# Optimization experiments

Measured on AMD Instinct MI355X. Metric: run time of the kernel, lower is better.

## Reference

```python
import jax, jax.numpy as jnp
import numpy as np

BLOCK = 64  # bitsandbytes 4-bit blocksize
OUT, IN = 4096, 4096
# NF4 codebook (bitsandbytes values)
NF4_CODE = np.array([
    -1.0, -0.6961928009986877, -0.5250730514526367, -0.39491748809814453,
    -0.28444138169288635, -0.18477343022823334, -0.09105003625154495, 0.0,
    0.07958029955625534, 0.16093020141124725, 0.24611230194568634,
    0.33791524171829224, 0.44070982933044434, 0.5626170039176941,
    0.7229568362236023, 1.0], dtype=np.float32)


def setup_inputs() -> dict:
    key = jax.random.key(0)
    k1, k2, k3 = jax.random.split(key, 3)
    x = jax.random.normal(k1, (8, 2048, IN), dtype=jnp.float32)
    qweight = jax.random.randint(k2, (OUT * IN,), 0, 16, dtype=jnp.int32)
    absmax = jax.random.uniform(k3, (OUT * IN // BLOCK,), dtype=jnp.float32)
    return {"x": x, "qweight": qweight, "absmax": absmax}


def reference(x, qweight, absmax):
    code = jnp.asarray(NF4_CODE)
    # dequantize: codebook lookup, then per-block absmax scaling
    w = code[qweight].reshape(-1, BLOCK) * absmax[:, None]  # [n_blocks, BLOCK]
    W = w.reshape(OUT, IN)                                   # [out, in]
    # linear: y = x @ W^T  (no bias: quantized_bias is None)
    return jnp.einsum('bsi,oi->bso', x, W)
```

## Files before the change

### kernel.cpp

```cpp
#include <hip/hip_runtime.h>
#include <hip/hip_bf16.h>
#include <stdint.h>

#define IN_DIM  4096
#define OUT_DIM 4096
#define M_DIM   16384
#define BK      64
#define NT      (IN_DIM / BK)

typedef float f32x4 __attribute__((ext_vector_type(4)));
typedef short bf16x8 __attribute__((ext_vector_type(8)));
typedef short bf16x4 __attribute__((ext_vector_type(4)));
typedef int   i32x4 __attribute__((ext_vector_type(4)));

__device__ __constant__ float NF4_CODE_D[16] = {
    -1.0f, -0.6961928009986877f, -0.5250730514526367f, -0.39491748809814453f,
    -0.28444138169288635f, -0.18477343022823334f, -0.09105003625154495f, 0.0f,
    0.07958029955625534f, 0.16093020141124725f, 0.24611230194568634f,
    0.33791524171829224f, 0.44070982933044434f, 0.5626170039176941f,
    0.7229568362236023f, 1.0f};

static __device__ __forceinline__ ushort f2bf(float f) {
  union { float f; uint32_t u; } v; v.f = f;
  uint32_t r = v.u + 0x7FFFu + ((v.u >> 16) & 1u);
  return (ushort)(r >> 16);
}

__global__ void dequant_nf4(const int* __restrict__ q, const float* __restrict__ am,
                            ushort* __restrict__ w) {
  __shared__ float code[16];
  if (threadIdx.x < 16) code[threadIdx.x] = NF4_CODE_D[threadIdx.x];
  __syncthreads();
  size_t t = (size_t)blockIdx.x * blockDim.x + threadIdx.x;
  size_t base = t * 8;
  i32x4 qa = *(const i32x4*)(q + base);
  i32x4 qb = *(const i32x4*)(q + base + 4);
  float s = am[base >> 6];
  bf16x8 o;
  o[0] = (short)f2bf(code[qa[0] & 15] * s);
  o[1] = (short)f2bf(code[qa[1] & 15] * s);
  o[2] = (short)f2bf(code[qa[2] & 15] * s);
  o[3] = (short)f2bf(code[qa[3] & 15] * s);
  o[4] = (short)f2bf(code[qb[0] & 15] * s);
  o[5] = (short)f2bf(code[qb[1] & 15] * s);
  o[6] = (short)f2bf(code[qb[2] & 15] * s);
  o[7] = (short)f2bf(code[qb[3] & 15] * s);
  *(bf16x8*)(w + base) = o;
}

__global__ void cvt_x(const float* __restrict__ x, ushort* __restrict__ xb) {
  size_t t = (size_t)blockIdx.x * blockDim.x + threadIdx.x;
  size_t base = t * 8;
  f32x4 a = *(const f32x4*)(x + base);
  f32x4 b = *(const f32x4*)(x + base + 4);
  bf16x8 o;
  o[0] = (short)f2bf(a[0]); o[1] = (short)f2bf(a[1]);
  o[2] = (short)f2bf(a[2]); o[3] = (short)f2bf(a[3]);
  o[4] = (short)f2bf(b[0]); o[5] = (short)f2bf(b[1]);
  o[6] = (short)f2bf(b[2]); o[7] = (short)f2bf(b[3]);
  *(bf16x8*)(xb + base) = o;
}

static __device__ __forceinline__ void llds16(const ushort* g, ushort* l) {
  __builtin_amdgcn_global_load_lds(
      (const __attribute__((address_space(1))) void*)g,
      (__attribute__((address_space(3))) void*)l, 16, 0, 0);
}

__global__ __launch_bounds__(512, 2) void gemm256(const ushort* __restrict__ Xb,
                                                  const ushort* __restrict__ W,
                                                  float* __restrict__ Y) {
  __shared__ ushort As[2][256 * BK];
  __shared__ ushort Bs[2][256 * BK];

  const int tid  = threadIdx.x;
  const int lane = tid & 63;
  const int wid  = tid >> 6;
  const int wr   = wid >> 2;
  const int wc   = wid & 3;
  const int l15  = lane & 15;
  const int kg   = lane >> 4;
  const int l7   = lane & 7;

  const int bid = blockIdx.x;
  const int wg  = (bid & 7) * 128 + (bid >> 3);
  const int tm  = wg >> 4;
  const int tn  = wg & 15;
  const size_t row0 = (size_t)tm * 256;
  const size_t col0 = (size_t)tn * 256;

  const int srow  = tid >> 3;
  const int scol8 = ((tid & 7) ^ (srow & 7)) * 8;
  const int wbase = wid << 9;

  f32x4  acc[8][4] = {};
  bf16x8 aA[4][2], aB[4][2], b0[2][2], b1[2][2];

#define BARX()   asm volatile("s_barrier" ::: "memory")
#define LGKM0()  do { asm volatile("s_waitcnt lgkmcnt(0)" ::: "memory"); \
                      __builtin_amdgcn_sched_barrier(0); } while (0)
#define LGKM8()  asm volatile("s_waitcnt lgkmcnt(8)" ::: "memory")
#define VMC(n)   asm volatile("s_waitcnt vmcnt(" #n ")" ::: "memory")
#define PRI1()   __builtin_amdgcn_s_setprio(1)
#define PRI0()   __builtin_amdgcn_s_setprio(0)

#define STAGE_A(kt, h, nb) do { \
    llds16(Xb + (row0 + (h)*128 +  0 + srow) * IN_DIM + (kt)*BK + scol8, \
           &As[nb][(h)*8192 +    0 + wbase]); \
    llds16(Xb + (row0 + (h)*128 + 64 + srow) * IN_DIM + (kt)*BK + scol8, \
           &As[nb][(h)*8192 + 4096 + wbase]); \
  } while (0)

#define STAGE_B(kt, h, nb) do { \
    llds16(W + (col0 + (h)*128 +  0 + srow) * IN_DIM + (kt)*BK + scol8, \
           &Bs[nb][(h)*8192 +    0 + wbase]); \
    llds16(W + (col0 + (h)*128 + 64 + srow) * IN_DIM + (kt)*BK + scol8, \
           &Bs[nb][(h)*8192 + 4096 + wbase]); \
  } while (0)

#define LDA_(dst, nb, mh) do { \
    _Pragma("unroll") for (int mi = 0; mi < 4; ++mi) \
    _Pragma("unroll") for (int ks = 0; ks < 2; ++ks) \
      dst[mi][ks] = *(const bf16x8*)&As[nb][((mh)*128 + wr*64 + mi*16 + l15) * BK \
                                            + (((ks*4 + kg) ^ l7) * 8)]; \
  } while (0)

#define LDB_(dst, nb, nh) do { \
    _Pragma("unroll") for (int ni = 0; ni < 2; ++ni) \
    _Pragma("unroll") for (int ks = 0; ks < 2; ++ks) \
      dst[ni][ks] = *(const bf16x8*)&Bs[nb][((nh)*128 + wc*32 + ni*16 + l15) * BK \
                                            + (((ks*4 + kg) ^ l7) * 8)]; \
  } while (0)

#define QUAD(mh, nh, aR, bR) do { PRI1(); \
    _Pragma("unroll") for (int mi = 0; mi < 4; ++mi) \
    _Pragma("unroll") for (int ni = 0; ni < 2; ++ni) \
    _Pragma("unroll") for (int ks = 0; ks < 2; ++ks) \
      acc[(mh)*4 + mi][(nh)*2 + ni] = __builtin_amdgcn_mfma_f32_16x16x32_bf16( \
          aR[mi][ks], bR[ni][ks], acc[(mh)*4 + mi][(nh)*2 + ni], 0, 0, 0); \
    PRI0(); } while (0)

  STAGE_A(0, 0, 0); STAGE_B(0, 0, 0); STAGE_A(0, 1, 0); STAGE_B(0, 1, 0);
  STAGE_A(1, 0, 1); STAGE_B(1, 0, 1); STAGE_A(1, 1, 1); STAGE_B(1, 1, 1);
  VMC(8); BARX();
  LDA_(aA, 0, 0); LDB_(b0, 0, 0);

#pragma unroll 1
  for (int t = 0; t < NT - 2; ++t) {
    const int cur = t & 1, nxt = cur ^ 1;
    LDA_(aB, cur, 1);
    STAGE_A(t + 2, 0, cur);
    BARX(); LGKM0();
    QUAD(0, 0, aA, b0);
    BARX();
    LDB_(b1, cur, 1);
    STAGE_B(t + 2, 0, cur);
    BARX(); LGKM0();
    QUAD(1, 0, aB, b0);
    BARX();
    STAGE_A(t + 2, 1, cur);
    VMC(10);
    BARX(); LGKM0();
    QUAD(0, 1, aA, b1);
    BARX();
    LDA_(aA, nxt, 0); LDB_(b0, nxt, 0);
    STAGE_B(t + 2, 1, cur);
    LGKM8();
    VMC(8);
    BARX(); LGKM0();
    QUAD(1, 1, aB, b1);
    BARX();
  }

  LDA_(aB, 0, 1);
  BARX(); LGKM0();
  QUAD(0, 0, aA, b0);
  BARX();
  LDB_(b1, 0, 1);
  BARX(); LGKM0();
  QUAD(1, 0, aB, b0);
  BARX();
  VMC(4);
  BARX(); LGKM0();
  QUAD(0, 1, aA, b1);
  BARX();
  LDA_(aA, 1, 0); LDB_(b0, 1, 0);
  LGKM8(); VMC(0);
  BARX(); LGKM0();
  QUAD(1, 1, aB, b1);
  BARX();

  LDA_(aB, 1, 1); LDB_(b1, 1, 1);
  QUAD(0, 0, aA, b0);
  QUAD(1, 0, aB, b0);
  QUAD(0, 1, aA, b1);
  QUAD(1, 1, aB, b1);

#undef QUAD
#undef LDB_
#undef LDA_
#undef STAGE_B
#undef STAGE_A

  float* yb = Y + (row0 + wr * 64 + kg * 4) * OUT_DIM + col0 + wc * 32 + l15;
#pragma unroll
  for (int mh = 0; mh < 2; ++mh)
#pragma unroll
    for (int mi = 0; mi < 4; ++mi)
#pragma unroll
      for (int nh = 0; nh < 2; ++nh)
#pragma unroll
        for (int ni = 0; ni < 2; ++ni)
#pragma unroll
          for (int v = 0; v < 4; ++v)
            yb[(size_t)(mh * 128 + mi * 16 + v) * OUT_DIM + nh * 128 + ni * 16] =
                acc[mh * 4 + mi][nh * 2 + ni][v];
}

__global__ void gemm_fb(const float* __restrict__ X, const ushort* __restrict__ W,
                        float* __restrict__ Y) {
  __shared__ ushort Af[128 * 64];
  __shared__ ushort Bf[128 * 64];
  const int tid  = threadIdx.x;
  const int lane = tid & 63;
  const int wid  = tid >> 6;
  const int wr   = wid >> 1, wc = wid & 1;
  const int bid  = blockIdx.x;
  const int tm   = bid / 32, tn = bid % 32;
  const size_t row0 = (size_t)tm * 128, col0 = (size_t)tn * 128;
  f32x4 acc[4][4] = {};
  const int arow = lane & 15, kgrp = lane >> 4;
  const int srow = lane >> 3, scol = (lane & 7) * 8;
  for (int k0 = 0; k0 < IN_DIM; k0 += 64) {
    f32x4 r[8];
#pragma unroll
    for (int i = 0; i < 8; ++i)
      r[i] = *(const f32x4*)(X + (row0 + i * 16 + (tid >> 4)) * IN_DIM + k0 + (tid & 15) * 4);
#pragma unroll
    for (int i = 0; i < 8; ++i) {
      bf16x4 o;
      o[0] = (short)f2bf(r[i][0]); o[1] = (short)f2bf(r[i][1]);
      o[2] = (short)f2bf(r[i][2]); o[3] = (short)f2bf(r[i][3]);
      *(bf16x4*)&Af[(i * 16 + (tid >> 4)) * 64 + (tid & 15) * 4] = o;
    }
#pragma unroll
    for (int i = 0; i < 4; ++i) {
      const int c = wid * 4 + i;
      llds16(W + (col0 + c * 8 + srow) * IN_DIM + k0 + scol, Bf + c * 512);
    }
    __syncthreads();
#pragma unroll
    for (int ks = 0; ks < 2; ++ks) {
      bf16x8 a[4], b[4];
#pragma unroll
      for (int m = 0; m < 4; ++m)
        a[m] = *(const bf16x8*)&Af[(wr * 64 + m * 16 + arow) * 64 + ks * 32 + kgrp * 8];
#pragma unroll
      for (int n = 0; n < 4; ++n)
        b[n] = *(const bf16x8*)&Bf[(wc * 64 + n * 16 + arow) * 64 + ks * 32 + kgrp * 8];
#pragma unroll
      for (int m = 0; m < 4; ++m)
#pragma unroll
        for (int n = 0; n < 4; ++n)
          acc[m][n] = __builtin_amdgcn_mfma_f32_16x16x32_bf16(a[m], b[n], acc[m][n], 0, 0, 0);
    }
    __syncthreads();
  }
  float* yb = Y + (row0 + wr * 64) * OUT_DIM + col0 + wc * 64;
  const int crow = (lane >> 4) * 4, ccol = lane & 15;
#pragma unroll
  for (int m = 0; m < 4; ++m)
#pragma unroll
    for (int n = 0; n < 4; ++n)
#pragma unroll
      for (int v = 0; v < 4; ++v)
        yb[(size_t)(m * 16 + crow + v) * OUT_DIM + n * 16 + ccol] = acc[m][n][v];
}

extern "C" void kernel_launch(void* const* d_in, const int* in_sizes, int n_in,
                              void* d_out, int out_size, void* d_ws, size_t ws_size,
                              hipStream_t stream) {
  const float* x  = (const float*)d_in[0];
  const int*   q  = (const int*)d_in[1];
  const float* am = (const float*)d_in[2];
  float* y = (float*)d_out;

  ushort* w = (ushort*)d_ws;
  const size_t WB = (size_t)OUT_DIM * IN_DIM * sizeof(ushort);
  const size_t XB = (size_t)M_DIM * IN_DIM * sizeof(ushort);

  dequant_nf4<<<(OUT_DIM * (size_t)IN_DIM) / 8 / 256, 256, 0, stream>>>(q, am, w);

  if (ws_size >= WB + XB) {
    ushort* xb = (ushort*)((char*)d_ws + WB);
    cvt_x<<<((size_t)M_DIM * IN_DIM) / 8 / 256, 256, 0, stream>>>(x, xb);
    gemm256<<<(M_DIM / 256) * (OUT_DIM / 256), 512, 0, stream>>>(xb, w, y);
  } else {
    gemm_fb<<<(M_DIM / 128) * (OUT_DIM / 128), 256, 0, stream>>>(x, w, y);
  }
}
```

Baseline: 616.3 us.

## Merge dequant and x-convert kernels, reschedule GEMM main-loop LDS/stage order

Combines the NF4 dequantization and fp32-to-bf16 conversion of x into one prep kernel, selected by block index, which removes a launch and lets the two phases overlap. It also reorders the GEMM main loop so that the four MFMA quadrants run in the order (0,0),(0,1),(1,0),(1,1). Fragment loads from LDS are moved into the current iteration, and the last B stage of the next tile is issued inside the loop, with adjusted vmcnt waits. The new schedule changes how global-to-LDS staging overlaps with compute, and it needs the wait counts to stay correct to avoid races.

```diff
diff --git a/kernel.cpp b/kernel.cpp
--- a/kernel.cpp
+++ b/kernel.cpp
@@ -26,39 +26,41 @@
   return (ushort)(r >> 16);
 }
 
-__global__ void dequant_nf4(const int* __restrict__ q, const float* __restrict__ am,
-                            ushort* __restrict__ w) {
-  __shared__ float code[16];
-  if (threadIdx.x < 16) code[threadIdx.x] = NF4_CODE_D[threadIdx.x];
-  __syncthreads();
-  size_t t = (size_t)blockIdx.x * blockDim.x + threadIdx.x;
-  size_t base = t * 8;
-  i32x4 qa = *(const i32x4*)(q + base);
-  i32x4 qb = *(const i32x4*)(q + base + 4);
-  float s = am[base >> 6];
-  bf16x8 o;
-  o[0] = (short)f2bf(code[qa[0] & 15] * s);
-  o[1] = (short)f2bf(code[qa[1] & 15] * s);
-  o[2] = (short)f2bf(code[qa[2] & 15] * s);
-  o[3] = (short)f2bf(code[qa[3] & 15] * s);
-  o[4] = (short)f2bf(code[qb[0] & 15] * s);
-  o[5] = (short)f2bf(code[qb[1] & 15] * s);
-  o[6] = (short)f2bf(code[qb[2] & 15] * s);
-  o[7] = (short)f2bf(code[qb[3] & 15] * s);
-  *(bf16x8*)(w + base) = o;
-}
-
-__global__ void cvt_x(const float* __restrict__ x, ushort* __restrict__ xb) {
-  size_t t = (size_t)blockIdx.x * blockDim.x + threadIdx.x;
-  size_t base = t * 8;
-  f32x4 a = *(const f32x4*)(x + base);
-  f32x4 b = *(const f32x4*)(x + base + 4);
-  bf16x8 o;
-  o[0] = (short)f2bf(a[0]); o[1] = (short)f2bf(a[1]);
-  o[2] = (short)f2bf(a[2]); o[3] = (short)f2bf(a[3]);
-  o[4] = (short)f2bf(b[0]); o[5] = (short)f2bf(b[1]);
-  o[6] = (short)f2bf(b[2]); o[7] = (short)f2bf(b[3]);
-  *(bf16x8*)(xb + base) = o;
+#define NB_W 8192
+__global__ void prep(const float* __restrict__ x, const int* __restrict__ q,
+                     const float* __restrict__ am, ushort* __restrict__ xb,
+                     ushort* __restrict__ w) {
+  if (blockIdx.x < NB_W) {
+    __shared__ float code[16];
+    if (threadIdx.x < 16) code[threadIdx.x] = NF4_CODE_D[threadIdx.x];
+    __syncthreads();
+    size_t t = (size_t)blockIdx.x * 256 + threadIdx.x;
+    size_t base = t * 8;
+    i32x4 qa = *(const i32x4*)(q + base);
+    i32x4 qb = *(const i32x4*)(q + base + 4);
+    float s = am[base >> 6];
+    bf16x8 o;
+    o[0] = (short)f2bf(code[qa[0] & 15] * s);
+    o[1] = (short)f2bf(code[qa[1] & 15] * s);
+    o[2] = (short)f2bf(code[qa[2] & 15] * s);
+    o[3] = (short)f2bf(code[qa[3] & 15] * s);
+    o[4] = (short)f2bf(code[qb[0] & 15] * s);
+    o[5] = (short)f2bf(code[qb[1] & 15] * s);
+    o[6] = (short)f2bf(code[qb[2] & 15] * s);
+    o[7] = (short)f2bf(code[qb[3] & 15] * s);
+    *(bf16x8*)(w + base) = o;
+  } else {
+    size_t t = (size_t)(blockIdx.x - NB_W) * 256 + threadIdx.x;
+    size_t base = t * 8;
+    f32x4 a = *(const f32x4*)(x + base);
+    f32x4 b = *(const f32x4*)(x + base + 4);
+    bf16x8 o;
+    o[0] = (short)f2bf(a[0]); o[1] = (short)f2bf(a[1]);
+    o[2] = (short)f2bf(a[2]); o[3] = (short)f2bf(a[3]);
+    o[4] = (short)f2bf(b[0]); o[5] = (short)f2bf(b[1]);
+    o[6] = (short)f2bf(b[2]); o[7] = (short)f2bf(b[3]);
+    *(bf16x8*)(xb + base) = o;
+  }
 }
 
 static __device__ __forceinline__ void llds16(const ushort* g, ushort* l) {
@@ -141,59 +143,60 @@
     PRI0(); } while (0)
 
   STAGE_A(0, 0, 0); STAGE_B(0, 0, 0); STAGE_A(0, 1, 0); STAGE_B(0, 1, 0);
-  STAGE_A(1, 0, 1); STAGE_B(1, 0, 1); STAGE_A(1, 1, 1); STAGE_B(1, 1, 1);
-  VMC(8); BARX();
-  LDA_(aA, 0, 0); LDB_(b0, 0, 0);
+  STAGE_A(1, 0, 1); STAGE_B(1, 0, 1); STAGE_A(1, 1, 1);
+  VMC(6); BARX();
 
 #pragma unroll 1
   for (int t = 0; t < NT - 2; ++t) {
     const int cur = t & 1, nxt = cur ^ 1;
-    LDA_(aB, cur, 1);
+    LDA_(aA, cur, 0); LDB_(b0, cur, 0);
+    STAGE_B(t + 1, 1, nxt);
+    LGKM8();
+    BARX(); LGKM0();
+    QUAD(0, 0, aA, b0);
+    BARX();
+    LDB_(b1, cur, 1);
     STAGE_A(t + 2, 0, cur);
     BARX(); LGKM0();
-    QUAD(0, 0, aA, b0);
-    BARX();
-    LDB_(b1, cur, 1);
+    QUAD(0, 1, aA, b1);
+    BARX();
+    LDA_(aB, cur, 1);
     STAGE_B(t + 2, 0, cur);
     BARX(); LGKM0();
     QUAD(1, 0, aB, b0);
     BARX();
     STAGE_A(t + 2, 1, cur);
-    VMC(10);
-    BARX(); LGKM0();
-    QUAD(0, 1, aA, b1);
-    BARX();
-    LDA_(aA, nxt, 0); LDB_(b0, nxt, 0);
-    STAGE_B(t + 2, 1, cur);
-    LGKM8();
-    VMC(8);
-    BARX(); LGKM0();
+    VMC(6);
+    BARX();
     QUAD(1, 1, aB, b1);
     BARX();
   }
 
+  LDA_(aA, 0, 0); LDB_(b0, 0, 0);
+  STAGE_B(NT - 1, 1, 1);
+  LGKM8();
+  BARX(); LGKM0();
+  QUAD(0, 0, aA, b0);
+  BARX();
+  LDB_(b1, 0, 1);
+  BARX(); LGKM0();
+  QUAD(0, 1, aA, b1);
+  BARX();
   LDA_(aB, 0, 1);
   BARX(); LGKM0();
+  QUAD(1, 0, aB, b0);
+  BARX();
+  VMC(0);
+  BARX();
+  QUAD(1, 1, aB, b1);
+  BARX();
+
+  LDA_(aA, 1, 0); LDB_(b0, 1, 0);
   QUAD(0, 0, aA, b0);
-  BARX();
-  LDB_(b1, 0, 1);
-  BARX(); LGKM0();
+  LDB_(b1, 1, 1);
+  QUAD(0, 1, aA, b1);
+  LDA_(aB, 1, 1);
   QUAD(1, 0, aB, b0);
-  BARX();
-  VMC(4);
-  BARX(); LGKM0();
-  QUAD(0, 1, aA, b1);
-  BARX();
-  LDA_(aA, 1, 0); LDB_(b0, 1, 0);
-  LGKM8(); VMC(0);
-  BARX(); LGKM0();
-  QUAD(1, 1, aB, b1);
-  BARX();
-
-  LDA_(aB, 1, 1); LDB_(b1, 1, 1);
-  QUAD(0, 0, aA, b0);
-  QUAD(1, 0, aB, b0);
-  QUAD(0, 1, aA, b1);
   QUAD(1, 1, aB, b1);
 
 #undef QUAD
@@ -289,13 +292,13 @@
   const size_t WB = (size_t)OUT_DIM * IN_DIM * sizeof(ushort);
   const size_t XB = (size_t)M_DIM * IN_DIM * sizeof(ushort);
 
-  dequant_nf4<<<(OUT_DIM * (size_t)IN_DIM) / 8 / 256, 256, 0, stream>>>(q, am, w);
-
   if (ws_size >= WB + XB) {
     ushort* xb = (ushort*)((char*)d_ws + WB);
-    cvt_x<<<((size_t)M_DIM * IN_DIM) / 8 / 256, 256, 0, stream>>>(x, xb);
+    const int nb = NB_W + (int)((size_t)M_DIM * IN_DIM / 8 / 256);
+    prep<<<nb, 256, 0, stream>>>(x, q, am, xb, w);
     gemm256<<<(M_DIM / 256) * (OUT_DIM / 256), 512, 0, stream>>>(xb, w, y);
   } else {
+    prep<<<NB_W, 256, 0, stream>>>(x, q, am, nullptr, w);
     gemm_fb<<<(M_DIM / 128) * (OUT_DIM / 128), 256, 0, stream>>>(x, w, y);
   }
 }
```

New measurement: 694.2 us. 12.6% more time.
